# Kernel tuning notes

Hardware: AMD Instinct MI355X
Metric: run time of the kernel (lower is better)

The kernel has to match this reference:

```python
import jax, jax.numpy as jnp
import numpy as np

B, S, F, H = 64, 2048, 1024, 1024

def setup_inputs() -> dict:
    key = jax.random.key(0)
    ks = jax.random.split(key, 16)
    inp = {
        "input": jax.random.normal(ks[0], (B,), jnp.float32),
        "hidden": jax.random.normal(ks[1], (1, B, H), jnp.float32),
        "encoder_outputs": jax.random.normal(ks[2], (B, S, F), jnp.float32),
        "attention_mask": jax.random.randint(ks[3], (B, S), 0, 2, jnp.int32),
    }
    s = lambda n: 1.0 / np.sqrt(n)
    inp["attn_W"] = jax.random.uniform(ks[4], (1, F + H + 1), jnp.float32, -s(F+H+1), s(F+H+1))
    inp["attn_b"] = jax.random.uniform(ks[5], (1,), jnp.float32, -s(F+H+1), s(F+H+1))
    inp["combine_W"] = jax.random.uniform(ks[6], (H, F + 1), jnp.float32, -s(F+1), s(F+1))
    inp["combine_b"] = jax.random.uniform(ks[7], (H,), jnp.float32, -s(F+1), s(F+1))
    inp["W_ih"] = jax.random.uniform(ks[8], (3 * H, H), jnp.float32, -s(H), s(H))
    inp["W_hh"] = jax.random.uniform(ks[9], (3 * H, H), jnp.float32, -s(H), s(H))
    inp["b_ih"] = jax.random.uniform(ks[10], (3 * H,), jnp.float32, -s(H), s(H))
    inp["b_hh"] = jax.random.uniform(ks[11], (3 * H,), jnp.float32, -s(H), s(H))
    inp["out_W"] = jax.random.uniform(ks[12], (1, H), jnp.float32, -s(H), s(H))
    inp["out_b"] = jax.random.uniform(ks[13], (1,), jnp.float32, -s(H), s(H))
    return inp


def reference(input, hidden, encoder_outputs, attention_mask,
              attn_W, attn_b, combine_W, combine_b,
              W_ih, W_hh, b_ih, b_hh, out_W, out_b):
    # Dropout in eval mode (identity); faithful to deterministic inference.
    h = hidden[0]                                   # [B, H]
    # Additive attention score: Linear over cat(enc, h_expanded, input_expanded)
    # is split into three partial matmuls (same math, no [B,S,F+H+1] concat).
    w_e = attn_W[0, :F]                             # [F]
    w_h = attn_W[0, F:F + H]                        # [H]
    w_i = attn_W[0, -1]                             # scalar
    scores = (jnp.einsum('bsf,f->bs', encoder_outputs, w_e)
              + (h @ w_h)[:, None]
              + input[:, None] * w_i
              + attn_b[0])                          # [B, S]
    scores = jnp.where(attention_mask == 0, jnp.float32(-1e10), scores)
    attn_weights = jax.nn.softmax(scores, axis=1)   # [B, S]
    attn_applied = jnp.einsum('bs,bsf->bf', attn_weights, encoder_outputs)  # [B, F]

    x = jnp.concatenate([input[:, None], attn_applied], axis=1)  # [B, F+1]
    x = jax.nn.relu(x @ combine_W.T + combine_b)    # [B, H]

    # Single GRU step (PyTorch gate order: r, z, n)
    gi = x @ W_ih.T + b_ih                          # [B, 3H]
    gh = h @ W_hh.T + b_hh                          # [B, 3H]
    r = jax.nn.sigmoid(gi[:, :H] + gh[:, :H])
    z = jax.nn.sigmoid(gi[:, H:2 * H] + gh[:, H:2 * H])
    n = jnp.tanh(gi[:, 2 * H:] + r * gh[:, 2 * H:])
    h_new = (1.0 - z) * n + z * h                   # [B, H]

    out = jax.nn.relu(h_new) @ out_W.T + out_b      # [B, 1]
    return out[:, 0], h_new[None], attn_weights[:, :, None]
```

## Files before the change

kernel.cpp:

```cpp
#include <hip/hip_runtime.h>
#include <math.h>

#define BB 64
#define SS 2048
#define FF 1024
#define HH 1024
#define NCHUNK 32
#define KSPLIT 8
#define KCH 128

#define WS_PL    0
#define WS_XT    2048
#define WS_X2T   (WS_XT+65536)
#define WS_EPART (WS_X2T+65536)
#define WS_GPART (WS_EPART+524288)
#define WS_PACC  (WS_GPART+3145728)

__device__ __forceinline__ float sigm(float x){ return 1.f/(1.f + __expf(-x)); }

__global__ __launch_bounds__(256) void kBH(const float* __restrict__ enc,
                                           const int*   __restrict__ mask,
                                           const float* __restrict__ attn_W,
                                           const float* __restrict__ input,
                                           const float* __restrict__ hidden,
                                           const float* __restrict__ attn_b,
                                           const float* __restrict__ W_hh,
                                           float* __restrict__ scores_out,
                                           float* __restrict__ pacc,
                                           float* __restrict__ pl,
                                           float* __restrict__ gpart)
{
    __shared__ __align__(16) char smem[16400];
    const int tid  = threadIdx.x;
    const int lane = tid & 63;
    const int w    = tid >> 6;

    if (blockIdx.x >= 2048){
        float* Wl = (float*)smem;
        int idx = blockIdx.x - 2048;
        int rb = idx >> 3, kc = idx & 7;
        int r0 = rb*16, k0 = kc*KCH;
        for (int t=tid; t<2048; t+=256){
            int row = t>>7, kk = t&127;
            Wl[t] = W_hh[(size_t)(r0+row)*HH + k0 + kk];
        }
        __syncthreads();
        float acc[4] = {0.f,0.f,0.f,0.f};
        const float* wp = Wl + (w*4)*KCH;
        const float4* hr = (const float4*)(hidden + (size_t)lane*HH + k0);
        for (int ks=0; ks<KCH; ks+=32){
            float4 hv4[8];
            #pragma unroll
            for (int q=0;q<8;++q) hv4[q] = hr[(ks>>2) + q];
            #pragma unroll
            for (int q=0;q<8;++q){
                int kk = ks + q*4;
                float h0 = hv4[q].x, h1 = hv4[q].y, h2 = hv4[q].z, h3 = hv4[q].w;
                #pragma unroll
                for (int jj=0;jj<4;jj++){
                    float4 wv = *(const float4*)(wp + jj*KCH + kk);
                    acc[jj] += h0*wv.x + h1*wv.y + h2*wv.z + h3*wv.w;
                }
            }
        }
        #pragma unroll
        for (int jj=0;jj<4;jj++)
            gpart[((size_t)kc*6*HH + 3*HH + r0 + w*4 + jj)*BB + lane] = acc[jj];
        return;
    }

    float4 (*sacc)[256] = (float4(*)[256])smem;
    float* sl = (float*)(smem + 16384);

    const int b    = blockIdx.x >> 5;
    const int c    = blockIdx.x & 31;
    const int s0   = c*64;

    const float4* we4 = (const float4*)attn_W;
    const float4 we0 = we4[lane], we1 = we4[64+lane], we2 = we4[128+lane], we3 = we4[192+lane];

    const float4* h4  = (const float4*)(hidden + (size_t)b*HH);
    const float4* wh4 = (const float4*)(attn_W + FF);
    float4 hv0 = h4[lane], hv1 = h4[64+lane], hv2 = h4[128+lane], hv3 = h4[192+lane];
    float4 wv0 = wh4[lane], wv1 = wh4[64+lane], wv2 = wh4[128+lane], wv3 = wh4[192+lane];
    float bp = hv0.x*wv0.x + hv0.y*wv0.y + hv0.z*wv0.z + hv0.w*wv0.w
             + hv1.x*wv1.x + hv1.y*wv1.y + hv1.z*wv1.z + hv1.w*wv1.w
             + hv2.x*wv2.x + hv2.y*wv2.y + hv2.z*wv2.z + hv2.w*wv2.w
             + hv3.x*wv3.x + hv3.y*wv3.y + hv3.z*wv3.z + hv3.w*wv3.w;
    #pragma unroll
    for (int off=32; off; off>>=1) bp += __shfl_xor(bp, off);
    const float bb = bp + input[b]*attn_W[FF+HH] + attn_b[0];

    int m = mask[b*SS + s0 + lane];
    unsigned long long v = __ballot(m != 0);
    int cnt = (int)__popcll(v);
    int share = (cnt + 3) >> 2;
    int start = w*share; if (start > cnt) start = cnt;
    int end = start + share; if (end > cnt) end = cnt;
    int mycount = end - start;

    unsigned long long vv = v;
    for (int i=0; i<start; ++i) vv &= vv - 1;

    const float4* encw = (const float4*)(enc + (size_t)(b*SS + s0)*FF);

    float l = 0.f;
    float4 a0 = make_float4(0,0,0,0), a1 = a0, a2 = a0, a3 = a0;
    float sc_keep = 0.f;
    unsigned long long written = 0ull;

    int npair = mycount >> 1;
    for (int p=0; p<npair; ++p){
        int rA = (int)__builtin_ctzll(vv); vv &= vv-1;
        int rB = (int)__builtin_ctzll(vv); vv &= vv-1;
        const float4* pA = encw + (size_t)rA*(FF/4);
        const float4* pB = encw + (size_t)rB*(FF/4);
        float4 e0 = pA[lane], e1 = pA[64+lane], e2 = pA[128+lane], e3 = pA[192+lane];
        float4 f0 = pB[lane], f1 = pB[64+lane], f2 = pB[128+lane], f3 = pB[192+lane];
        float da = (e0.x*we0.x + e0.y*we0.y + e0.z*we0.z + e0.w*we0.w)
                 + (e1.x*we1.x + e1.y*we1.y + e1.z*we1.z + e1.w*we1.w)
                 + (e2.x*we2.x + e2.y*we2.y + e2.z*we2.z + e2.w*we2.w)
                 + (e3.x*we3.x + e3.y*we3.y + e3.z*we3.z + e3.w*we3.w);
        float db = (f0.x*we0.x + f0.y*we0.y + f0.z*we0.z + f0.w*we0.w)
                 + (f1.x*we1.x + f1.y*we1.y + f1.z*we1.z + f1.w*we1.w)
                 + (f2.x*we2.x + f2.y*we2.y + f2.z*we2.z + f2.w*we2.w)
                 + (f3.x*we3.x + f3.y*we3.y + f3.z*we3.z + f3.w*we3.w);
        #pragma unroll
        for (int off=32; off; off>>=1){ da += __shfl_xor(da, off); db += __shfl_xor(db, off); }
        float scA = da + bb, scB = db + bb;
        float pAe = __expf(scA), pBe = __expf(scB);
        l += pAe + pBe;
        a0.x += pAe*e0.x + pBe*f0.x; a0.y += pAe*e0.y + pBe*f0.y; a0.z += pAe*e0.z + pBe*f0.z; a0.w += pAe*e0.w + pBe*f0.w;
        a1.x += pAe*e1.x + pBe*f1.x; a1.y += pAe*e1.y + pBe*f1.y; a1.z += pAe*e1.z + pBe*f1.z; a1.w += pAe*e1.w + pBe*f1.w;
        a2.x += pAe*e2.x + pBe*f2.x; a2.y += pAe*e2.y + pBe*f2.y; a2.z += pAe*e2.z + pBe*f2.z; a2.w += pAe*e2.w + pBe*f2.w;
        a3.x += pAe*e3.x + pBe*f3.x; a3.y += pAe*e3.y + pBe*f3.y; a3.z += pAe*e3.z + pBe*f3.z; a3.w += pAe*e3.w + pBe*f3.w;
        sc_keep = (lane == rA) ? scA : sc_keep;
        sc_keep = (lane == rB) ? scB : sc_keep;
        written |= (1ull << rA) | (1ull << rB);
    }
    if (mycount & 1){
        int rA = (int)__builtin_ctzll(vv);
        const float4* pA = encw + (size_t)rA*(FF/4);
        float4 e0 = pA[lane], e1 = pA[64+lane], e2 = pA[128+lane], e3 = pA[192+lane];
        float da = (e0.x*we0.x + e0.y*we0.y + e0.z*we0.z + e0.w*we0.w)
                 + (e1.x*we1.x + e1.y*we1.y + e1.z*we1.z + e1.w*we1.w)
                 + (e2.x*we2.x + e2.y*we2.y + e2.z*we2.z + e2.w*we2.w)
                 + (e3.x*we3.x + e3.y*we3.y + e3.z*we3.z + e3.w*we3.w);
        #pragma unroll
        for (int off=32; off; off>>=1) da += __shfl_xor(da, off);
        float scA = da + bb;
        float pAe = __expf(scA);
        l += pAe;
        a0.x += pAe*e0.x; a0.y += pAe*e0.y; a0.z += pAe*e0.z; a0.w += pAe*e0.w;
        a1.x += pAe*e1.x; a1.y += pAe*e1.y; a1.z += pAe*e1.z; a1.w += pAe*e1.w;
        a2.x += pAe*e2.x; a2.y += pAe*e2.y; a2.z += pAe*e2.z; a2.w += pAe*e2.w;
        a3.x += pAe*e3.x; a3.y += pAe*e3.y; a3.z += pAe*e3.z; a3.w += pAe*e3.w;
        sc_keep = (lane == rA) ? scA : sc_keep;
        written |= (1ull << rA);
    }
    if ((written >> lane) & 1ull) scores_out[b*SS + s0 + lane] = sc_keep;
    if (w == 0 && m == 0)         scores_out[b*SS + s0 + lane] = -1e10f;

    if (lane==0) sl[w] = l;
    sacc[w][lane]     = a0;
    sacc[w][64+lane]  = a1;
    sacc[w][128+lane] = a2;
    sacc[w][192+lane] = a3;
    __syncthreads();
    float4 tot = sacc[0][tid];
    #pragma unroll
    for (int q=1;q<4;q++){ float4 u = sacc[q][tid]; tot.x+=u.x; tot.y+=u.y; tot.z+=u.z; tot.w+=u.w; }
    ((float4*)(pacc + (size_t)blockIdx.x*FF))[tid] = tot;
    if (tid==0) pl[blockIdx.x] = sl[0]+sl[1]+sl[2]+sl[3];
}

__global__ __launch_bounds__(256) void kC(const float* __restrict__ pacc,
                                          const float* __restrict__ pl,
                                          const float* __restrict__ out_b,
                                          float* __restrict__ xT,
                                          float* __restrict__ wout,
                                          float* __restrict__ out)
{
    int b = blockIdx.x >> 2, q = blockIdx.x & 3, tid = threadIdx.x;
    float L = 0.f;
    #pragma unroll
    for (int c=0;c<NCHUNK;c++) L += pl[b*NCHUNK+c];
    float invL = 1.f/L;

    int f = q*256 + tid;
    float a = 0.f;
    #pragma unroll
    for (int c=0;c<NCHUNK;c++) a += pacc[((size_t)(b*NCHUNK+c))*FF + f];
    xT[(size_t)f*BB + b] = a*invL;

    if (q == 0){
        for (int t = tid; t < SS; t += 256){
            int idx2 = b*SS + t;
            wout[idx2] = __expf(wout[idx2]) * invL;
        }
    } else if (q == 1){
        if (tid == 0) out[b] = out_b[0];
    }
}

__global__ __launch_bounds__(256) void kE1(const float* __restrict__ xT,
                                           const float* __restrict__ cW,
                                           float* __restrict__ epart)
{
    __shared__ __align__(16) float Wl[16*KCH];
    int tid = threadIdx.x, lane = tid&63, w = tid>>6;
    int jb = blockIdx.x >> 3, kc = blockIdx.x & 7;
    int j0 = jb*16, k0 = kc*KCH;

    for (int idx=tid; idx<16*KCH; idx+=256){
        int row = idx>>7, kk = idx&127;
        Wl[idx] = cW[(size_t)(j0+row)*(FF+1) + 1 + k0 + kk];
    }
    __syncthreads();

    float acc[4] = {0.f,0.f,0.f,0.f};
    const float* wp = Wl + (w*4)*KCH;
    for (int ks=0; ks<KCH; ks+=32){
        float xv[32];
        #pragma unroll
        for (int i=0;i<32;++i) xv[i] = xT[(size_t)(k0+ks+i)*BB + lane];
        #pragma unroll
        for (int q=0;q<8;++q){
            int kk = ks + q*4;
            float x0 = xv[q*4+0], x1 = xv[q*4+1], x2 = xv[q*4+2], x3 = xv[q*4+3];
            #pragma unroll
            for (int jj=0;jj<4;jj++){
                float4 wv = *(const float4*)(wp + jj*KCH + kk);
                acc[jj] += x0*wv.x + x1*wv.y + x2*wv.z + x3*wv.w;
            }
        }
    }
    #pragma unroll
    for (int jj=0;jj<4;jj++)
        epart[((size_t)kc*HH + j0 + w*4 + jj)*BB + lane] = acc[jj];
}

__global__ __launch_bounds__(256) void kE2(const float* __restrict__ epart,
                                           const float* __restrict__ input,
                                           const float* __restrict__ cW,
                                           const float* __restrict__ cb,
                                           float* __restrict__ x2T)
{
    int tid = threadIdx.x, lane = tid&63, w = tid>>6;
    int j = blockIdx.x*4 + w;
    float s = 0.f;
    #pragma unroll
    for (int kc=0;kc<KSPLIT;kc++) s += epart[((size_t)kc*HH + j)*BB + lane];
    s += input[lane]*cW[(size_t)j*(FF+1)] + cb[j];
    x2T[(size_t)j*BB + lane] = fmaxf(s, 0.f);
}

__global__ __launch_bounds__(256) void kF1(const float* __restrict__ x2T,
                                           const float* __restrict__ W_ih,
                                           float* __restrict__ gpart)
{
    __shared__ __align__(16) float Wl[16*KCH];
    int tid = threadIdx.x, lane = tid&63, w = tid>>6;
    int rb = blockIdx.x >> 3, kc = blockIdx.x & 7;
    int r0 = rb*16, k0 = kc*KCH;

    for (int t=tid; t<16*KCH; t+=256){
        int row = t>>7, kk = t&127;
        Wl[t] = W_ih[(size_t)(r0+row)*HH + k0 + kk];
    }
    __syncthreads();

    float acc[4] = {0.f,0.f,0.f,0.f};
    const float* wp = Wl + (w*4)*KCH;
    for (int ks=0; ks<KCH; ks+=32){
        float xv[32];
        #pragma unroll
        for (int i=0;i<32;++i) xv[i] = x2T[(size_t)(k0+ks+i)*BB + lane];
        #pragma unroll
        for (int q=0;q<8;++q){
            int kk = ks + q*4;
            float x0 = xv[q*4+0], x1 = xv[q*4+1], x2 = xv[q*4+2], x3 = xv[q*4+3];
            #pragma unroll
            for (int jj=0;jj<4;jj++){
                float4 wv = *(const float4*)(wp + jj*KCH + kk);
                acc[jj] += x0*wv.x + x1*wv.y + x2*wv.z + x3*wv.w;
            }
        }
    }
    #pragma unroll
    for (int jj=0;jj<4;jj++)
        gpart[((size_t)kc*6*HH + r0 + w*4 + jj)*BB + lane] = acc[jj];
}

__global__ __launch_bounds__(256) void kF2(const float* __restrict__ gpart,
                                           const float* __restrict__ b_ih,
                                           const float* __restrict__ b_hh,
                                           const float* __restrict__ hidden,
                                           const float* __restrict__ out_W,
                                           float* __restrict__ hnew,
                                           float* __restrict__ out)
{
    int tid = threadIdx.x, lane = tid&63, w = tid>>6;
    int j = blockIdx.x*4 + w;
    float g[6];
    #pragma unroll
    for (int gi=0; gi<6; gi++){
        int row = (gi < 3) ? (gi*HH + j) : (3*HH + (gi-3)*HH + j);
        float s = 0.f;
        #pragma unroll
        for (int kc=0;kc<KSPLIT;kc++) s += gpart[((size_t)kc*6*HH + row)*BB + lane];
        g[gi] = s;
    }
    float r = sigm(g[0]+b_ih[j]        + g[3]+b_hh[j]);
    float z = sigm(g[1]+b_ih[HH+j]     + g[4]+b_hh[HH+j]);
    float n = tanhf(g[2]+b_ih[2*HH+j]  + r*(g[5]+b_hh[2*HH+j]));
    float hold = hidden[(size_t)lane*HH + j];
    float hn = (1.f - z)*n + z*hold;
    hnew[(size_t)lane*HH + j] = hn;
    float pv = fmaxf(hn, 0.f) * out_W[j];
    __shared__ float red[4][64];
    red[w][lane] = pv;
    __syncthreads();
    if (w==0) atomicAdd(out + lane, red[0][lane]+red[1][lane]+red[2][lane]+red[3][lane]);
}

extern "C" void kernel_launch(void* const* d_in, const int* in_sizes, int n_in,
                              void* d_out, int out_size, void* d_ws, size_t ws_size,
                              hipStream_t stream) {
    const float* input     = (const float*)d_in[0];
    const float* hidden    = (const float*)d_in[1];
    const float* enc       = (const float*)d_in[2];
    const int*   mask      = (const int*)  d_in[3];
    const float* attn_W    = (const float*)d_in[4];
    const float* attn_b    = (const float*)d_in[5];
    const float* combine_W = (const float*)d_in[6];
    const float* combine_b = (const float*)d_in[7];
    const float* W_ih      = (const float*)d_in[8];
    const float* W_hh      = (const float*)d_in[9];
    const float* b_ih      = (const float*)d_in[10];
    const float* b_hh      = (const float*)d_in[11];
    const float* out_W     = (const float*)d_in[12];
    const float* out_b     = (const float*)d_in[13];

    float* out  = (float*)d_out;
    float* hnew = out + 64;
    float* attw = out + 64 + BB*HH;
    float* ws   = (float*)d_ws;

    kBH<<<BB*NCHUNK + 1536, 256, 0, stream>>>(enc, mask, attn_W, input, hidden, attn_b,
                                              W_hh, attw, ws+WS_PACC, ws+WS_PL, ws+WS_GPART);
    kC <<<256,  256, 0, stream>>>(ws+WS_PACC, ws+WS_PL, out_b, ws+WS_XT, attw, out);
    kE1<<<512,  256, 0, stream>>>(ws+WS_XT, combine_W, ws+WS_EPART);
    kE2<<<256,  256, 0, stream>>>(ws+WS_EPART, input, combine_W, combine_b, ws+WS_X2T);
    kF1<<<1536, 256, 0, stream>>>(ws+WS_X2T, W_ih, ws+WS_GPART);
    kF2<<<256,  256, 0, stream>>>(ws+WS_GPART, b_ih, b_hh, hidden, out_W, hnew, out);
}
```

Before: 118.5 us.

## Stage activations in LDS for GEMV kernels, reorder blocks, transpose hidden

The W_hh partial-GEMM blocks now come first in the fused attention/W_hh launch, so they are scheduled ahead of the streaming attention blocks. In kE1 and kF1 the activation tile (128x64) is copied into shared memory once per block rather than read per lane from global memory, and kF1 now loads its W_ih tile with float4 reads. kC additionally writes a transposed copy of hidden so the GRU epilogue reads the old state coalesced. These changes cost 32KB more LDS per block, which may lower occupancy, and add an extra transpose pass.

```diff
diff --git a/kernel.cpp b/kernel.cpp
--- a/kernel.cpp
+++ b/kernel.cpp
@@ -8,10 +8,12 @@
 #define NCHUNK 32
 #define KSPLIT 8
 #define KCH 128
+#define NWHH 1536
 
 #define WS_PL    0
 #define WS_XT    2048
-#define WS_X2T   (WS_XT+65536)
+#define WS_HT    (WS_XT+65536)
+#define WS_X2T   (WS_HT+65536)
 #define WS_EPART (WS_X2T+65536)
 #define WS_GPART (WS_EPART+524288)
 #define WS_PACC  (WS_GPART+3145728)
@@ -35,9 +37,9 @@
     const int lane = tid & 63;
     const int w    = tid >> 6;
 
-    if (blockIdx.x >= 2048){
+    if (blockIdx.x < NWHH){
         float* Wl = (float*)smem;
-        int idx = blockIdx.x - 2048;
+        int idx = blockIdx.x;
         int rb = idx >> 3, kc = idx & 7;
         int r0 = rb*16, k0 = kc*KCH;
         for (int t=tid; t<2048; t+=256){
@@ -72,8 +74,9 @@
     float4 (*sacc)[256] = (float4(*)[256])smem;
     float* sl = (float*)(smem + 16384);
 
-    const int b    = blockIdx.x >> 5;
-    const int c    = blockIdx.x & 31;
+    const int idx_b = blockIdx.x - NWHH;
+    const int b    = idx_b >> 5;
+    const int c    = idx_b & 31;
     const int s0   = c*64;
 
     const float4* we4 = (const float4*)attn_W;
@@ -170,15 +173,17 @@
     float4 tot = sacc[0][tid];
     #pragma unroll
     for (int q=1;q<4;q++){ float4 u = sacc[q][tid]; tot.x+=u.x; tot.y+=u.y; tot.z+=u.z; tot.w+=u.w; }
-    ((float4*)(pacc + (size_t)blockIdx.x*FF))[tid] = tot;
-    if (tid==0) pl[blockIdx.x] = sl[0]+sl[1]+sl[2]+sl[3];
+    ((float4*)(pacc + (size_t)idx_b*FF))[tid] = tot;
+    if (tid==0) pl[idx_b] = sl[0]+sl[1]+sl[2]+sl[3];
 }
 
 __global__ __launch_bounds__(256) void kC(const float* __restrict__ pacc,
                                           const float* __restrict__ pl,
+                                          const float* __restrict__ hidden,
                                           const float* __restrict__ out_b,
                                           float* __restrict__ xT,
                                           float* __restrict__ wout,
+                                          float* __restrict__ hT,
                                           float* __restrict__ out)
 {
     int b = blockIdx.x >> 2, q = blockIdx.x & 3, tid = threadIdx.x;
@@ -199,6 +204,8 @@
             wout[idx2] = __expf(wout[idx2]) * invL;
         }
     } else if (q == 1){
+        for (int k = tid; k < HH; k += 256) hT[(size_t)k*BB + b] = hidden[(size_t)b*HH + k];
+    } else if (q == 2){
         if (tid == 0) out[b] = out_b[0];
     }
 }
@@ -207,11 +214,16 @@
                                            const float* __restrict__ cW,
                                            float* __restrict__ epart)
 {
+    __shared__ __align__(16) float Xl[KCH*64];
     __shared__ __align__(16) float Wl[16*KCH];
     int tid = threadIdx.x, lane = tid&63, w = tid>>6;
     int jb = blockIdx.x >> 3, kc = blockIdx.x & 7;
     int j0 = jb*16, k0 = kc*KCH;
 
+    const float4* xs = (const float4*)(xT + (size_t)k0*BB);
+    float4* xd = (float4*)Xl;
+    #pragma unroll
+    for (int r=tid; r<KCH*16; r+=256) xd[r] = xs[r];
     for (int idx=tid; idx<16*KCH; idx+=256){
         int row = idx>>7, kk = idx&127;
         Wl[idx] = cW[(size_t)(j0+row)*(FF+1) + 1 + k0 + kk];
@@ -220,19 +232,13 @@
 
     float acc[4] = {0.f,0.f,0.f,0.f};
     const float* wp = Wl + (w*4)*KCH;
-    for (int ks=0; ks<KCH; ks+=32){
-        float xv[32];
-        #pragma unroll
-        for (int i=0;i<32;++i) xv[i] = xT[(size_t)(k0+ks+i)*BB + lane];
-        #pragma unroll
-        for (int q=0;q<8;++q){
-            int kk = ks + q*4;
-            float x0 = xv[q*4+0], x1 = xv[q*4+1], x2 = xv[q*4+2], x3 = xv[q*4+3];
-            #pragma unroll
-            for (int jj=0;jj<4;jj++){
-                float4 wv = *(const float4*)(wp + jj*KCH + kk);
-                acc[jj] += x0*wv.x + x1*wv.y + x2*wv.z + x3*wv.w;
-            }
+    for (int kk=0; kk<KCH; kk+=4){
+        float x0 = Xl[kk*64+lane], x1 = Xl[(kk+1)*64+lane];
+        float x2 = Xl[(kk+2)*64+lane], x3 = Xl[(kk+3)*64+lane];
+        #pragma unroll
+        for (int jj=0;jj<4;jj++){
+            float4 wv = *(const float4*)(wp + jj*KCH + kk);
+            acc[jj] += x0*wv.x + x1*wv.y + x2*wv.z + x3*wv.w;
         }
     }
     #pragma unroll
@@ -259,32 +265,33 @@
                                            const float* __restrict__ W_ih,
                                            float* __restrict__ gpart)
 {
+    __shared__ __align__(16) float Xl[KCH*64];
     __shared__ __align__(16) float Wl[16*KCH];
     int tid = threadIdx.x, lane = tid&63, w = tid>>6;
     int rb = blockIdx.x >> 3, kc = blockIdx.x & 7;
     int r0 = rb*16, k0 = kc*KCH;
 
-    for (int t=tid; t<16*KCH; t+=256){
-        int row = t>>7, kk = t&127;
-        Wl[t] = W_ih[(size_t)(r0+row)*HH + k0 + kk];
+    const float4* xs = (const float4*)(x2T + (size_t)k0*BB);
+    float4* xd = (float4*)Xl;
+    #pragma unroll
+    for (int r=tid; r<KCH*16; r+=256) xd[r] = xs[r];
+    float4* wd = (float4*)Wl;
+    #pragma unroll
+    for (int idx4=tid; idx4<16*KCH/4; idx4+=256){
+        int row = idx4>>5, kq = idx4&31;
+        wd[idx4] = *(const float4*)(W_ih + (size_t)(r0+row)*HH + k0 + kq*4);
     }
     __syncthreads();
 
     float acc[4] = {0.f,0.f,0.f,0.f};
     const float* wp = Wl + (w*4)*KCH;
-    for (int ks=0; ks<KCH; ks+=32){
-        float xv[32];
-        #pragma unroll
-        for (int i=0;i<32;++i) xv[i] = x2T[(size_t)(k0+ks+i)*BB + lane];
-        #pragma unroll
-        for (int q=0;q<8;++q){
-            int kk = ks + q*4;
-            float x0 = xv[q*4+0], x1 = xv[q*4+1], x2 = xv[q*4+2], x3 = xv[q*4+3];
-            #pragma unroll
-            for (int jj=0;jj<4;jj++){
-                float4 wv = *(const float4*)(wp + jj*KCH + kk);
-                acc[jj] += x0*wv.x + x1*wv.y + x2*wv.z + x3*wv.w;
-            }
+    for (int kk=0; kk<KCH; kk+=4){
+        float x0 = Xl[kk*64+lane], x1 = Xl[(kk+1)*64+lane];
+        float x2 = Xl[(kk+2)*64+lane], x3 = Xl[(kk+3)*64+lane];
+        #pragma unroll
+        for (int jj=0;jj<4;jj++){
+            float4 wv = *(const float4*)(wp + jj*KCH + kk);
+            acc[jj] += x0*wv.x + x1*wv.y + x2*wv.z + x3*wv.w;
         }
     }
     #pragma unroll
@@ -295,7 +302,7 @@
 __global__ __launch_bounds__(256) void kF2(const float* __restrict__ gpart,
                                            const float* __restrict__ b_ih,
                                            const float* __restrict__ b_hh,
-                                           const float* __restrict__ hidden,
+                                           const float* __restrict__ hT,
                                            const float* __restrict__ out_W,
                                            float* __restrict__ hnew,
                                            float* __restrict__ out)
@@ -314,7 +321,7 @@
     float r = sigm(g[0]+b_ih[j]        + g[3]+b_hh[j]);
     float z = sigm(g[1]+b_ih[HH+j]     + g[4]+b_hh[HH+j]);
     float n = tanhf(g[2]+b_ih[2*HH+j]  + r*(g[5]+b_hh[2*HH+j]));
-    float hold = hidden[(size_t)lane*HH + j];
+    float hold = hT[(size_t)j*BB + lane];
     float hn = (1.f - z)*n + z*hold;
     hnew[(size_t)lane*HH + j] = hn;
     float pv = fmaxf(hn, 0.f) * out_W[j];
@@ -347,11 +354,12 @@
     float* attw = out + 64 + BB*HH;
     float* ws   = (float*)d_ws;
 
-    kBH<<<BB*NCHUNK + 1536, 256, 0, stream>>>(enc, mask, attn_W, input, hidden, attn_b,
+    kBH<<<NWHH + BB*NCHUNK, 256, 0, stream>>>(enc, mask, attn_W, input, hidden, attn_b,
                                               W_hh, attw, ws+WS_PACC, ws+WS_PL, ws+WS_GPART);
-    kC <<<256,  256, 0, stream>>>(ws+WS_PACC, ws+WS_PL, out_b, ws+WS_XT, attw, out);
+    kC <<<256,  256, 0, stream>>>(ws+WS_PACC, ws+WS_PL, hidden, out_b,
+                                  ws+WS_XT, attw, ws+WS_HT, out);
     kE1<<<512,  256, 0, stream>>>(ws+WS_XT, combine_W, ws+WS_EPART);
     kE2<<<256,  256, 0, stream>>>(ws+WS_EPART, input, combine_W, combine_b, ws+WS_X2T);
     kF1<<<1536, 256, 0, stream>>>(ws+WS_X2T, W_ih, ws+WS_GPART);
-    kF2<<<256,  256, 0, stream>>>(ws+WS_GPART, b_ih, b_hh, hidden, out_W, hnew, out);
-}
+    kF2<<<256,  256, 0, stream>>>(ws+WS_GPART, b_ih, b_hh, ws+WS_HT, out_W, hnew, out);
+}
```

After: 114.4 us. 3.5% less time.
